# Kernel tuning notes

Hardware: AMD Instinct MI355X
Metric: run time of the kernel (lower is better)

## Reference

```python
import jax, jax.numpy as jnp
import numpy as np

IN_DIM = 64
HIDDEN = 128
NUM_LAYERS = 2
N_NODES = 10000
N_EDGES = 160000
N_GRAPHS = 32


def _lin_params(key, fan_in, fan_out):
    kw, kb = jax.random.split(key)
    s = 1.0 / np.sqrt(fan_in)
    W = jax.random.uniform(kw, (fan_in, fan_out), jnp.float32, -s, s)
    b = jax.random.uniform(kb, (fan_out,), jnp.float32, -s, s)
    return W, b


def setup_inputs() -> dict:
    key = jax.random.key(0)
    ks = jax.random.split(key, 24)
    H = HIDDEN
    inp = {}
    inp["x1"] = jax.random.normal(ks[0], (N_NODES, IN_DIM), jnp.float32)
    inp["edge_index1"] = jax.random.randint(ks[1], (2, N_EDGES), 0, N_NODES)
    inp["batch1"] = jnp.sort(jax.random.randint(ks[2], (N_NODES,), 0, N_GRAPHS))
    inp["x2"] = jax.random.normal(ks[3], (N_NODES, IN_DIM), jnp.float32)
    inp["edge_index2"] = jax.random.randint(ks[4], (2, N_EDGES), 0, N_NODES)
    inp["batch2"] = jnp.sort(jax.random.randint(ks[5], (N_NODES,), 0, N_GRAPHS))
    # embedding: Linear(in_dim -> hidden)
    inp["W_emb"], inp["b_emb"] = _lin_params(ks[6], IN_DIM, H)
    # per-layer GEMBConv params, stacked over layers
    mW1, mb1, mW2, mb2, uW1, ub1, uW2, ub2 = [], [], [], [], [], [], [], []
    for l in range(NUM_LAYERS):
        k = jax.random.split(ks[7 + l], 4)
        W, b = _lin_params(k[0], 2 * H, 2 * H); mW1.append(W); mb1.append(b)
        W, b = _lin_params(k[1], 2 * H, 2 * H); mW2.append(W); mb2.append(b)
        W, b = _lin_params(k[2], 3 * H, 2 * H); uW1.append(W); ub1.append(b)
        W, b = _lin_params(k[3], 2 * H, H); uW2.append(W); ub2.append(b)
    inp["msg_W1"] = jnp.stack(mW1); inp["msg_b1"] = jnp.stack(mb1)
    inp["msg_W2"] = jnp.stack(mW2); inp["msg_b2"] = jnp.stack(mb2)
    inp["upd_W1"] = jnp.stack(uW1); inp["upd_b1"] = jnp.stack(ub1)
    inp["upd_W2"] = jnp.stack(uW2); inp["upd_b2"] = jnp.stack(ub2)
    # readout: node_net Linear(H -> 2H) (use_gate doubles), graph_net Linear(H -> H)
    inp["node_W"], inp["node_b"] = _lin_params(ks[20], H, 2 * H)
    inp["graph_W"], inp["graph_b"] = _lin_params(ks[21], H, H)
    return inp


def _genet_branch(x, edge_index, batch, W_emb, b_emb,
                  msg_W1, msg_b1, msg_W2, msg_b2,
                  upd_W1, upd_b1, upd_W2, upd_b2,
                  node_W, node_b, graph_W, graph_b):
    H = HIDDEN
    h = x @ W_emb + b_emb  # [N, H]
    tgt, src = edge_index[0], edge_index[1]
    for l in range(NUM_LAYERS):
        # gather-concat: (x[src], x[tgt]) -> [E, 2H]
        mi = jnp.concatenate([h[src], h[tgt]], axis=-1)
        m = jax.nn.relu(mi @ msg_W1[l] + msg_b1[l]) @ msg_W2[l] + msg_b2[l]
        agg = jax.ops.segment_sum(m, tgt, num_segments=N_NODES)  # [N, 2H]
        ui = jnp.concatenate([agg, h], axis=-1)  # [N, 3H]
        u = jax.nn.relu(ui @ upd_W1[l] + upd_b1[l]) @ upd_W2[l] + upd_b2[l]
        h = h + u  # residual node update
    nx = h @ node_W + node_b  # [N, 2H]
    gates = jax.nn.sigmoid(nx[:, :H])
    v = nx[:, H:] * gates
    g = jax.ops.segment_sum(v, batch, num_segments=N_GRAPHS)  # sum pool
    return g @ graph_W + graph_b  # [G, H]


def reference(x1, edge_index1, batch1, x2, edge_index2, batch2,
              W_emb, b_emb, msg_W1, msg_b1, msg_W2, msg_b2,
              upd_W1, upd_b1, upd_W2, upd_b2,
              node_W, node_b, graph_W, graph_b):
    args = (W_emb, b_emb, msg_W1, msg_b1, msg_W2, msg_b2,
            upd_W1, upd_b1, upd_W2, upd_b2, node_W, node_b, graph_W, graph_b)
    embed1 = _genet_branch(x1, edge_index1, batch1, *args)
    embed2 = _genet_branch(x2, edge_index2, batch2, *args)
    return (embed1, embed2)
```

## Files before the change

### kernel.cpp

```cpp
#include <hip/hip_runtime.h>

typedef unsigned short u16;
typedef __bf16 bf16x8 __attribute__((ext_vector_type(8)));
typedef float f32x4 __attribute__((ext_vector_type(4)));
typedef unsigned short u16x8 __attribute__((ext_vector_type(8)));

constexpr int NN  = 10000;
constexpr int NE  = 160000;
constexpr int NG  = 32;
constexpr int HD  = 128;

constexpr size_t WT_PQ   = 0;
constexpr size_t WT_U1C  = 917504;
constexpr size_t WT_UPD2 = 1310720;
constexpr size_t WT_NODE = 1441792;
constexpr size_t OFF_C2  = 1507328;
constexpr size_t OFF_DEG = 1509376;
constexpr size_t OFF_ST  = 1589376;
constexpr size_t OFF_CUR = 1669440;
constexpr size_t OFF_SRC = 1749440;
constexpr size_t OFF_H   = 3029440;
constexpr size_t OFF_HB  = 13269440;
constexpr size_t OFF_PQ  = 18389440;
constexpr size_t OFF_UI  = 38869440;
constexpr size_t OFF_G   = 54229440;
constexpr size_t OFF_XB  = 54262208;
constexpr size_t WT_EMB  = 56822208;

#define LSTR 40

__device__ inline u16 f2b(float f) {
  unsigned int u = __float_as_uint(f);
  unsigned int r = u + 0x7fffu + ((u >> 16) & 1u);
  return (u16)(r >> 16);
}
__device__ inline float b2f(u16 u) { return __uint_as_float(((unsigned int)u) << 16); }

__global__ __launch_bounds__(256) void k_prep(
    const float* msgW1, const float* msgW2, const float* updW1,
    const float* updW2, const float* nodeW, const float* msgb2,
    const float* W_emb, const float* x1, const float* x2,
    u16* tpq, u16* tu1c, u16* t4, u16* t5, u16* temb, u16* xb,
    float* c2, int* deg, float* g) {
  int idx = blockIdx.x * 256 + threadIdx.x;
  if (idx < 131072) {
    int l = idx >> 16, r = idx & 65535, n = r >> 7, k = r & 127;
    int row = (n < 256) ? k : (128 + k);
    tpq[idx] = f2b(msgW1[l * 65536 + row * 256 + (n & 255)]);
  }
  if (idx < 65536) {
    int l = idx >> 15, r = idx & 32767, n = r >> 7, k = r & 127;
    tu1c[l * 98304 + n * 384 + 256 + k] = f2b(updW1[l * 98304 + (256 + k) * 256 + n]);
    int n2 = (idx & 32767) >> 8, k2 = idx & 255;
    t4[idx] = f2b(updW2[(idx >> 15) * 32768 + (k2 << 7) + n2]);
  }
  if (idx < 32768) {
    int n = idx >> 7, k = idx & 127;
    t5[idx] = f2b(nodeW[(k << 8) + n]);
  }
  if (idx < 512) {
    int l = idx >> 8, n = idx & 255;
    const float* b2 = msgb2 + l * 256;
    const float* U1 = updW1 + l * 98304 + n;
    float a = 0.f;
    for (int c = 0; c < 256; c++) a += b2[c] * U1[c * 256];
    c2[idx] = a;
  }
  if (idx < 2 * NN) deg[idx] = 0;
  if (idx < 2 * NG * 128) g[idx] = 0.f;
  if (idx >= 131072 && idx < 262144) {
    int j = idx - 131072;
    int l = j >> 16, r = j & 65535, k = r >> 8, n = r & 255;
    const float* w2p = msgW2 + l * 65536 + k * 256;
    const float* u1p = updW1 + l * 98304 + n;
    float a = 0.f;
    for (int c = 0; c < 256; c++) a += w2p[c] * u1p[c * 256];
    tu1c[l * 98304 + n * 384 + k] = f2b(a);
  }
  if (idx >= 262144 && idx < 270336) {
    int j = idx - 262144;
    int n = j >> 6, k = j & 63;
    temb[j] = f2b(W_emb[(k << 7) + n]);
  }
  if (idx >= 270336 && idx < 1550336) {
    int j = idx - 270336;
    int br = j >= NN * 64;
    int jj = br ? j - NN * 64 : j;
    const float* x = br ? x2 : x1;
    xb[(size_t)br * NN * 64 + jj] = f2b(x[jj]);
  }
}

__global__ __launch_bounds__(256) void k_deg(const int* ei0, const int* ei1, int* deg) {
  int br = blockIdx.z;
  int e = blockIdx.x * 256 + threadIdx.x;
  if (e >= NE) return;
  const int* tgt = br ? ei1 : ei0;
  atomicAdd(deg + br * NN + tgt[e], 1);
}

__global__ __launch_bounds__(256) void k_scan(const int* deg, int* starts, int* cursor) {
  int br = blockIdx.z;
  const int* d = deg + br * NN;
  int* st = starts + br * (NN + 8);
  int* cu = cursor + br * NN;
  __shared__ int part[257];
  int t = threadIdx.x;
  int c0 = t * 40;
  int s = 0;
  for (int i = 0; i < 40; i++) if (c0 + i < NN) s += d[c0 + i];
  part[t] = s;
  __syncthreads();
  if (t == 0) {
    int run = 0;
    for (int i = 0; i < 256; i++) { int v = part[i]; part[i] = run; run += v; }
    part[256] = run;
  }
  __syncthreads();
  int run = part[t];
  for (int i = 0; i < 40; i++) {
    int n = c0 + i;
    if (n < NN) { st[n] = run; cu[n] = run; run += d[n]; }
  }
  if (t == 255) st[NN] = part[256];
}

__global__ __launch_bounds__(256) void k_scatter(const int* ei0, const int* ei1,
                                                 int* cursor, int* srcs) {
  int br = blockIdx.z;
  int e = blockIdx.x * 256 + threadIdx.x;
  if (e >= NE) return;
  const int* ei = br ? ei1 : ei0;
  int t = ei[e], s = ei[NE + e];
  int pos = atomicAdd(cursor + br * NN + t, 1);
  srcs[br * NE + pos] = s;
}

__device__ __forceinline__ void pq_from_lhb(
    const u16* lhb, const u16* wq, u16* PQ, int m0, int wave, int lane) {
  const int q = lane >> 4, lr = lane & 15;
  f32x4 a3[2][8];
#pragma unroll
  for (int i = 0; i < 2; i++)
#pragma unroll
    for (int j = 0; j < 8; j++) a3[i][j] = (f32x4){0.f, 0.f, 0.f, 0.f};
  bf16x8 bcur[8], bnxt[8];
#pragma unroll
  for (int i = 0; i < 8; i++)
    bcur[i] = *(const bf16x8*)(wq + (size_t)(wave * 128 + i * 16 + lr) * 128 + q * 8);
#pragma unroll
  for (int k0 = 0; k0 < 128; k0 += 32) {
    if (k0 + 32 < 128) {
#pragma unroll
      for (int i = 0; i < 8; i++)
        bnxt[i] = *(const bf16x8*)(wq + (size_t)(wave * 128 + i * 16 + lr) * 128 + k0 + 32 + q * 8);
    }
    bf16x8 af[2];
#pragma unroll
    for (int i = 0; i < 2; i++)
      af[i] = *(const bf16x8*)&lhb[(i * 16 + lr) * 136 + k0 + q * 8];
#pragma unroll
    for (int mi = 0; mi < 2; mi++)
#pragma unroll
      for (int ni = 0; ni < 8; ni++)
        a3[mi][ni] = __builtin_amdgcn_mfma_f32_16x16x32_bf16(af[mi], bcur[ni], a3[mi][ni], 0, 0, 0);
#pragma unroll
    for (int i = 0; i < 8; i++) bcur[i] = bnxt[i];
  }
#pragma unroll
  for (int mi = 0; mi < 2; mi++)
#pragma unroll
    for (int rg = 0; rg < 4; rg++) {
      int grow = m0 + mi * 16 + q * 4 + rg;
      if (grow >= NN) continue;
#pragma unroll
      for (int ni = 0; ni < 8; ni++) {
        int col = wave * 128 + ni * 16 + lr;
        PQ[(size_t)grow * 512 + col] = f2b(a3[mi][ni][rg]);
      }
    }
}

__global__ __launch_bounds__(256) void k_embed(
    const u16* xb_all, const u16* wemb, const float* b,
    float* h, u16* h_bf, u16* ui, const u16* wpq0, u16* PQ_all) {
  const int br = blockIdx.z;
  const int tid = threadIdx.x;
  const int lane = tid & 63, wave = tid >> 6;
  const int q = lane >> 4, lr = lane & 15;
  const int m0 = blockIdx.x * 32;

  __shared__ alignas(16) u16 lx[32 * 72];
  __shared__ alignas(16) u16 lhb[32 * 136];

  const u16* xb = xb_all + (size_t)br * NN * 64;
  {
    int r = tid >> 3, kc = (tid & 7) * 8;
    int gr = m0 + r;
    u16x8 v = {0, 0, 0, 0, 0, 0, 0, 0};
    if (gr < NN) v = *(const u16x8*)(xb + (size_t)gr * 64 + kc);
    *(u16x8*)&lx[r * 72 + kc] = v;
  }
  __syncthreads();

  const int wn = wave * 32;
  f32x4 acc[2][2];
#pragma unroll
  for (int i = 0; i < 2; i++)
#pragma unroll
    for (int j = 0; j < 2; j++) acc[i][j] = (f32x4){0.f, 0.f, 0.f, 0.f};

#pragma unroll
  for (int k0 = 0; k0 < 64; k0 += 32) {
    bf16x8 af[2], bfr[2];
#pragma unroll
    for (int i = 0; i < 2; i++)
      af[i] = *(const bf16x8*)&lx[(i * 16 + lr) * 72 + k0 + q * 8];
#pragma unroll
    for (int i = 0; i < 2; i++)
      bfr[i] = *(const bf16x8*)(wemb + (size_t)(wn + i * 16 + lr) * 64 + k0 + q * 8);
#pragma unroll
    for (int mi = 0; mi < 2; mi++)
#pragma unroll
      for (int ni = 0; ni < 2; ni++)
        acc[mi][ni] = __builtin_amdgcn_mfma_f32_16x16x32_bf16(af[mi], bfr[ni], acc[mi][ni], 0, 0, 0);
  }

  float* hB = h + (size_t)br * NN * HD;
  u16* hbB = h_bf + (size_t)br * NN * HD;
  u16* uiB = ui + (size_t)br * NN * 384;
#pragma unroll
  for (int mi = 0; mi < 2; mi++)
#pragma unroll
    for (int rg = 0; rg < 4; rg++) {
      int lrow = mi * 16 + q * 4 + rg;
      int gr = m0 + lrow;
#pragma unroll
      for (int ni = 0; ni < 2; ni++) {
        int col = wn + ni * 16 + lr;
        if (gr < NN) {
          float nh = acc[mi][ni][rg] + b[col];
          u16 bv = f2b(nh);
          hB[(size_t)gr * HD + col] = nh;
          hbB[(size_t)gr * HD + col] = bv;
          uiB[(size_t)gr * 384 + 256 + col] = bv;
          lhb[lrow * 136 + col] = bv;
        } else {
          lhb[lrow * 136 + col] = 0;
        }
      }
    }
  __syncthreads();
  pq_from_lhb(lhb, wpq0, PQ_all + (size_t)br * NN * 512, m0, wave, lane);
}

__global__ __launch_bounds__(256) void k_edge(const u16* PQ, const int* starts,
                                              const int* srcs, const float* b1, u16* ui) {
  int br = blockIdx.z;
  int node = blockIdx.x * 4 + (threadIdx.x >> 6);
  int lane = threadIdx.x & 63;
  int half = lane >> 5;
  int c0 = (lane & 31) * 8;
  const u16* PQb = PQ + (size_t)br * NN * 512;
  const int* st = starts + br * (NN + 8);
  const int* sr = srcs + br * NE;
  u16x8 qr = *(const u16x8*)(PQb + (size_t)node * 512 + 256 + c0);
  float qv[8], acc[8];
#pragma unroll
  for (int j = 0; j < 8; j++) { qv[j] = b2f(qr[j]) + b1[c0 + j]; acc[j] = 0.f; }
  int e0 = st[node], e1 = st[node + 1];
  int mid = e0 + ((e1 - e0 + 1) >> 1);
  int e = half ? mid : e0;
  int ee = half ? e1 : mid;
  for (; e + 3 < ee; e += 4) {
    int s0 = sr[e], s1 = sr[e + 1], s2 = sr[e + 2], s3 = sr[e + 3];
    u16x8 p0 = *(const u16x8*)(PQb + (size_t)s0 * 512 + c0);
    u16x8 p1 = *(const u16x8*)(PQb + (size_t)s1 * 512 + c0);
    u16x8 p2 = *(const u16x8*)(PQb + (size_t)s2 * 512 + c0);
    u16x8 p3 = *(const u16x8*)(PQb + (size_t)s3 * 512 + c0);
#pragma unroll
    for (int j = 0; j < 8; j++) {
      float v0 = b2f(p0[j]) + qv[j];
      float v1 = b2f(p1[j]) + qv[j];
      float v2 = b2f(p2[j]) + qv[j];
      float v3 = b2f(p3[j]) + qv[j];
      acc[j] += (v0 > 0.f ? v0 : 0.f) + (v1 > 0.f ? v1 : 0.f)
              + (v2 > 0.f ? v2 : 0.f) + (v3 > 0.f ? v3 : 0.f);
    }
  }
  for (; e + 1 < ee; e += 2) {
    int s0 = sr[e], s1 = sr[e + 1];
    u16x8 p0 = *(const u16x8*)(PQb + (size_t)s0 * 512 + c0);
    u16x8 p1 = *(const u16x8*)(PQb + (size_t)s1 * 512 + c0);
#pragma unroll
    for (int j = 0; j < 8; j++) {
      float v0 = b2f(p0[j]) + qv[j];
      float v1 = b2f(p1[j]) + qv[j];
      acc[j] += (v0 > 0.f ? v0 : 0.f) + (v1 > 0.f ? v1 : 0.f);
    }
  }
  if (e < ee) {
    int s0 = sr[e];
    u16x8 p0 = *(const u16x8*)(PQb + (size_t)s0 * 512 + c0);
#pragma unroll
    for (int j = 0; j < 8; j++) {
      float v0 = b2f(p0[j]) + qv[j];
      acc[j] += (v0 > 0.f ? v0 : 0.f);
    }
  }
#pragma unroll
  for (int j = 0; j < 8; j++) acc[j] += __shfl_xor(acc[j], 32);
  if (half == 0) {
    u16x8 o;
#pragma unroll
    for (int j = 0; j < 8; j++) o[j] = f2b(acc[j]);
    *(u16x8*)(ui + (size_t)br * NN * 384 + (size_t)node * 384 + c0) = o;
  }
}

__global__ __launch_bounds__(256, 4) void k_upd(
    const u16* ui_all, const u16* w1c, const float* b1u, const float* c2l,
    const int* deg_all, const u16* w2, const float* b2u,
    float* h_all, u16* hb_all, int mode,
    const u16* wpq_next, u16* PQ_all,
    const u16* wnode, const float* nb, const int* b0v, const int* b1v, float* g) {
  const int br = blockIdx.z;
  const int tid = threadIdx.x;
  const int lane = tid & 63, wave = tid >> 6;
  const int q = lane >> 4, lr = lane & 15;
  const int m0 = blockIdx.x * 32;

  __shared__ alignas(16) u16 lA[32 * 392];
  __shared__ alignas(16) u16 lhb[32 * 136];
  __shared__ int sbat[32];
  u16* lU = lA;

  const u16* ui = ui_all + (size_t)br * NN * 384;

  for (int c = tid; c < 1536; c += 256) {
    int r = c / 48, kc = (c % 48) * 8;
    int gr = m0 + r;
    u16x8 v = {0, 0, 0, 0, 0, 0, 0, 0};
    if (gr < NN) v = *(const u16x8*)(ui + (size_t)gr * 384 + kc);
    *(u16x8*)&lA[r * 392 + kc] = v;
  }
  if (mode == 1 && tid < 32) {
    const int* batch = br ? b1v : b0v;
    int n = m0 + tid;
    sbat[tid] = (n < NN) ? batch[n] : -1;
  }
  __syncthreads();

  const int wn = wave * 64;
  f32x4 acc[2][4];
#pragma unroll
  for (int i = 0; i < 2; i++)
#pragma unroll
    for (int j = 0; j < 4; j++) acc[i][j] = (f32x4){0.f, 0.f, 0.f, 0.f};

  bf16x8 bcur[4], bnxt[4];
#pragma unroll
  for (int i = 0; i < 4; i++)
    bcur[i] = *(const bf16x8*)(w1c + (size_t)(wn + i * 16 + lr) * 384 + q * 8);
#pragma unroll
  for (int k0 = 0; k0 < 384; k0 += 32) {
    if (k0 + 32 < 384) {
#pragma unroll
      for (int i = 0; i < 4; i++)
        bnxt[i] = *(const bf16x8*)(w1c + (size_t)(wn + i * 16 + lr) * 384 + k0 + 32 + q * 8);
    }
    bf16x8 af[2];
#pragma unroll
    for (int i = 0; i < 2; i++)
      af[i] = *(const bf16x8*)&lA[(i * 16 + lr) * 392 + k0 + q * 8];
#pragma unroll
    for (int mi = 0; mi < 2; mi++)
#pragma unroll
      for (int ni = 0; ni < 4; ni++)
        acc[mi][ni] = __builtin_amdgcn_mfma_f32_16x16x32_bf16(af[mi], bcur[ni], acc[mi][ni], 0, 0, 0);
#pragma unroll
    for (int i = 0; i < 4; i++) bcur[i] = bnxt[i];
  }
  __syncthreads();

  const int* deg = deg_all + br * NN;
#pragma unroll
  for (int mi = 0; mi < 2; mi++)
#pragma unroll
    for (int rg = 0; rg < 4; rg++) {
      int row = mi * 16 + q * 4 + rg;
      int gr = m0 + row;
      float d = (gr < NN) ? (float)deg[gr] : 0.f;
#pragma unroll
      for (int ni = 0; ni < 4; ni++) {
        int col = wn + ni * 16 + lr;
        float v = acc[mi][ni][rg] + b1u[col] + d * c2l[col];
        if (v < 0.f) v = 0.f;
        lU[row * 272 + col] = f2b(v);
      }
    }
  __syncthreads();

  const int wn2 = wave * 32;
  f32x4 acc2[2][2];
#pragma unroll
  for (int i = 0; i < 2; i++)
#pragma unroll
    for (int j = 0; j < 2; j++) acc2[i][j] = (f32x4){0.f, 0.f, 0.f, 0.f};

  bf16x8 b2c[2], b2n[2];
#pragma unroll
  for (int i = 0; i < 2; i++)
    b2c[i] = *(const bf16x8*)(w2 + (size_t)(wn2 + i * 16 + lr) * 256 + q * 8);
#pragma unroll
  for (int k0 = 0; k0 < 256; k0 += 32) {
    if (k0 + 32 < 256) {
#pragma unroll
      for (int i = 0; i < 2; i++)
        b2n[i] = *(const bf16x8*)(w2 + (size_t)(wn2 + i * 16 + lr) * 256 + k0 + 32 + q * 8);
    }
    bf16x8 af[2];
#pragma unroll
    for (int i = 0; i < 2; i++)
      af[i] = *(const bf16x8*)&lU[(i * 16 + lr) * 272 + k0 + q * 8];
#pragma unroll
    for (int mi = 0; mi < 2; mi++)
#pragma unroll
      for (int ni = 0; ni < 2; ni++)
        acc2[mi][ni] = __builtin_amdgcn_mfma_f32_16x16x32_bf16(af[mi], b2c[ni], acc2[mi][ni], 0, 0, 0);
#pragma unroll
    for (int i = 0; i < 2; i++) b2c[i] = b2n[i];
  }

  float* h = h_all + (size_t)br * NN * 128;
  u16* hb = hb_all + (size_t)br * NN * 128;
  u16* uiw = (u16*)ui_all + (size_t)br * NN * 384;
#pragma unroll
  for (int mi = 0; mi < 2; mi++)
#pragma unroll
    for (int rg = 0; rg < 4; rg++) {
      int lrow = mi * 16 + q * 4 + rg;
      int grow = m0 + lrow;
#pragma unroll
      for (int ni = 0; ni < 2; ni++) {
        int col = wn2 + ni * 16 + lr;
        if (grow < NN) {
          size_t o = (size_t)grow * 128 + col;
          float nh = h[o] + acc2[mi][ni][rg] + b2u[col];
          u16 bv = f2b(nh);
          h[o] = nh;
          hb[o] = bv;
          uiw[(size_t)grow * 384 + 256 + col] = bv;
          lhb[lrow * 136 + col] = bv;
        } else {
          lhb[lrow * 136 + col] = 0;
        }
      }
    }
  __syncthreads();

  if (mode == 0) {
    pq_from_lhb(lhb, wpq_next, PQ_all + (size_t)br * NN * 512, m0, wave, lane);
  } else {
    const int wg = wave * 32;
    f32x4 a3[2][4];
#pragma unroll
    for (int i = 0; i < 2; i++)
#pragma unroll
      for (int j = 0; j < 4; j++) a3[i][j] = (f32x4){0.f, 0.f, 0.f, 0.f};
#pragma unroll
    for (int k0 = 0; k0 < 128; k0 += 32) {
      bf16x8 af[2], bfr[4];
#pragma unroll
      for (int i = 0; i < 2; i++)
        af[i] = *(const bf16x8*)&lhb[(i * 16 + lr) * 136 + k0 + q * 8];
#pragma unroll
      for (int i = 0; i < 4; i++) {
        int nrow = (i < 2) ? (wg + i * 16 + lr) : (128 + wg + (i - 2) * 16 + lr);
        bfr[i] = *(const bf16x8*)(wnode + (size_t)nrow * 128 + k0 + q * 8);
      }
#pragma unroll
      for (int mi = 0; mi < 2; mi++)
#pragma unroll
        for (int ni = 0; ni < 4; ni++)
          a3[mi][ni] = __builtin_amdgcn_mfma_f32_16x16x32_bf16(af[mi], bfr[ni], a3[mi][ni], 0, 0, 0);
    }
    float* gb = g + (size_t)br * NG * 128;
    float racc[2] = {0.f, 0.f};
    int cur = -1;
#pragma unroll
    for (int mi = 0; mi < 2; mi++)
#pragma unroll
      for (int rg = 0; rg < 4; rg++) {
        int lrow = mi * 16 + q * 4 + rg;
        int bt = sbat[lrow];
        if (bt != cur) {
          if (cur >= 0) {
#pragma unroll
            for (int ni = 0; ni < 2; ni++)
              atomicAdd(gb + (size_t)cur * 128 + wg + ni * 16 + lr, racc[ni]);
          }
          cur = bt;
          racc[0] = 0.f; racc[1] = 0.f;
        }
        if (bt >= 0) {
#pragma unroll
          for (int ni = 0; ni < 2; ni++) {
            int gcol = wg + ni * 16 + lr;
            float gt = a3[mi][ni][rg] + nb[gcol];
            float vl = a3[mi][ni + 2][rg] + nb[128 + gcol];
            racc[ni] += vl / (1.f + __expf(-gt));
          }
        }
      }
    if (cur >= 0) {
#pragma unroll
      for (int ni = 0; ni < 2; ni++)
        atomicAdd(gb + (size_t)cur * 128 + wg + ni * 16 + lr, racc[ni]);
    }
  }
}

__global__ __launch_bounds__(128) void k_final(const float* g, const float* W,
                                               const float* b, float* out) {
  int br = blockIdx.z, gi = blockIdx.x, j = threadIdx.x;
  __shared__ float sg[128];
  sg[j] = g[(size_t)br * NG * 128 + (size_t)gi * 128 + j];
  __syncthreads();
  float acc = b[j];
#pragma unroll
  for (int k = 0; k < 128; k++) acc += sg[k] * W[k * 128 + j];
  out[(size_t)br * NG * 128 + (size_t)gi * 128 + j] = acc;
}

extern "C" void kernel_launch(void* const* d_in, const int* in_sizes, int n_in,
                              void* d_out, int out_size, void* d_ws, size_t ws_size,
                              hipStream_t stream) {
  const float* x1     = (const float*)d_in[0];
  const int*   ei1    = (const int*)d_in[1];
  const int*   bat1   = (const int*)d_in[2];
  const float* x2     = (const float*)d_in[3];
  const int*   ei2    = (const int*)d_in[4];
  const int*   bat2   = (const int*)d_in[5];
  const float* W_emb  = (const float*)d_in[6];
  const float* b_emb  = (const float*)d_in[7];
  const float* msg_W1 = (const float*)d_in[8];
  const float* msg_b1 = (const float*)d_in[9];
  const float* msg_W2 = (const float*)d_in[10];
  const float* msg_b2 = (const float*)d_in[11];
  const float* upd_W1 = (const float*)d_in[12];
  const float* upd_b1 = (const float*)d_in[13];
  const float* upd_W2 = (const float*)d_in[14];
  const float* upd_b2 = (const float*)d_in[15];
  const float* node_W = (const float*)d_in[16];
  const float* node_b = (const float*)d_in[17];
  const float* graph_W = (const float*)d_in[18];
  const float* graph_b = (const float*)d_in[19];
  float* out = (float*)d_out;

  char* ws = (char*)d_ws;
  u16* wt_pq   = (u16*)(ws + WT_PQ);
  u16* wt_u1c  = (u16*)(ws + WT_U1C);
  u16* wt_upd2 = (u16*)(ws + WT_UPD2);
  u16* wt_node = (u16*)(ws + WT_NODE);
  u16* wt_emb  = (u16*)(ws + WT_EMB);
  u16* xb      = (u16*)(ws + OFF_XB);
  float* c2    = (float*)(ws + OFF_C2);
  int* deg    = (int*)(ws + OFF_DEG);
  int* starts = (int*)(ws + OFF_ST);
  int* cursor = (int*)(ws + OFF_CUR);
  int* srcs   = (int*)(ws + OFF_SRC);
  float* h  = (float*)(ws + OFF_H);
  u16*   hb = (u16*)(ws + OFF_HB);
  u16*   PQ = (u16*)(ws + OFF_PQ);
  u16*   ui = (u16*)(ws + OFF_UI);
  float* g  = (float*)(ws + OFF_G);

  k_prep<<<6057, 256, 0, stream>>>(msg_W1, msg_W2, upd_W1, upd_W2, node_W, msg_b2,
                                   W_emb, x1, x2,
                                   wt_pq, wt_u1c, wt_upd2, wt_node, wt_emb, xb,
                                   c2, deg, g);
  k_deg<<<dim3(625, 1, 2), 256, 0, stream>>>(ei1, ei2, deg);
  k_scan<<<dim3(1, 1, 2), 256, 0, stream>>>(deg, starts, cursor);
  k_scatter<<<dim3(625, 1, 2), 256, 0, stream>>>(ei1, ei2, cursor, srcs);
  k_embed<<<dim3(313, 1, 2), 256, 0, stream>>>(xb, wt_emb, b_emb, h, hb, ui,
                                               wt_pq, PQ);

  for (int l = 0; l < 2; l++) {
    k_edge<<<dim3(2500, 1, 2), 256, 0, stream>>>(PQ, starts, srcs, msg_b1 + l * 256, ui);

    k_upd<<<dim3(313, 1, 2), 256, 0, stream>>>(
        ui, wt_u1c + (size_t)l * 98304, upd_b1 + l * 256, c2 + l * 256,
        deg, wt_upd2 + (size_t)l * 32768, upd_b2 + l * 128, h, hb,
        (l == 0) ? 0 : 1,
        wt_pq + 65536, PQ,
        wt_node, node_b, bat1, bat2, g);
  }

  k_final<<<dim3(NG, 1, 2), 128, 0, stream>>>(g, graph_W, graph_b, out);
}
```

Before: 331.8 us.

## Split node update into tiled GEMM kernel plus fused second-stage kernel

Result: slower. 345.9 us (+4.2%).

```diff
diff --git a/kernel.cpp b/kernel.cpp
--- a/kernel.cpp
+++ b/kernel.cpp
@@ -26,6 +26,7 @@
 constexpr size_t OFF_G   = 54229440;
 constexpr size_t OFF_XB  = 54262208;
 constexpr size_t WT_EMB  = 56822208;
+constexpr size_t OFF_U1  = 56838592;
 
 #define LSTR 40
 
@@ -144,28 +145,20 @@
   for (int i = 0; i < 2; i++)
 #pragma unroll
     for (int j = 0; j < 8; j++) a3[i][j] = (f32x4){0.f, 0.f, 0.f, 0.f};
-  bf16x8 bcur[8], bnxt[8];
-#pragma unroll
-  for (int i = 0; i < 8; i++)
-    bcur[i] = *(const bf16x8*)(wq + (size_t)(wave * 128 + i * 16 + lr) * 128 + q * 8);
 #pragma unroll
   for (int k0 = 0; k0 < 128; k0 += 32) {
-    if (k0 + 32 < 128) {
-#pragma unroll
-      for (int i = 0; i < 8; i++)
-        bnxt[i] = *(const bf16x8*)(wq + (size_t)(wave * 128 + i * 16 + lr) * 128 + k0 + 32 + q * 8);
-    }
-    bf16x8 af[2];
+    bf16x8 af[2], bfr[8];
 #pragma unroll
     for (int i = 0; i < 2; i++)
       af[i] = *(const bf16x8*)&lhb[(i * 16 + lr) * 136 + k0 + q * 8];
 #pragma unroll
+    for (int i = 0; i < 8; i++)
+      bfr[i] = *(const bf16x8*)(wq + (size_t)(wave * 128 + i * 16 + lr) * 128 + k0 + q * 8);
+#pragma unroll
     for (int mi = 0; mi < 2; mi++)
 #pragma unroll
       for (int ni = 0; ni < 8; ni++)
-        a3[mi][ni] = __builtin_amdgcn_mfma_f32_16x16x32_bf16(af[mi], bcur[ni], a3[mi][ni], 0, 0, 0);
-#pragma unroll
-    for (int i = 0; i < 8; i++) bcur[i] = bnxt[i];
+        a3[mi][ni] = __builtin_amdgcn_mfma_f32_16x16x32_bf16(af[mi], bfr[ni], a3[mi][ni], 0, 0, 0);
   }
 #pragma unroll
   for (int mi = 0; mi < 2; mi++)
@@ -318,93 +311,107 @@
   }
 }
 
-__global__ __launch_bounds__(256, 4) void k_upd(
+__global__ __launch_bounds__(256) void k_upd1(
     const u16* ui_all, const u16* w1c, const float* b1u, const float* c2l,
-    const int* deg_all, const u16* w2, const float* b2u,
-    float* h_all, u16* hb_all, int mode,
+    const int* deg_all, u16* U1_all) {
+  const int br = blockIdx.z;
+  const int tid = threadIdx.x;
+  const int lane = tid & 63, wave = tid >> 6;
+  const int wm = (wave & 1) * 64, wn = (wave >> 1) * 64;
+  const int q = lane >> 4, lr = lane & 15;
+  const int m0 = blockIdx.x * 128, n0 = blockIdx.y * 128;
+  __shared__ alignas(16) u16 lA[128 * LSTR];
+  __shared__ alignas(16) u16 lB[128 * LSTR];
+
+  f32x4 acc[4][4];
+#pragma unroll
+  for (int i = 0; i < 4; i++)
+#pragma unroll
+    for (int j = 0; j < 4; j++) acc[i][j] = (f32x4){0.f, 0.f, 0.f, 0.f};
+
+  const u16* ui = ui_all + (size_t)br * NN * 384;
+
+  for (int k0 = 0; k0 < 384; k0 += 32) {
+#pragma unroll
+    for (int c = tid; c < 512; c += 256) {
+      int r = c >> 2, kc = (c & 3) << 3;
+      int gr = m0 + r;
+      u16x8 v = {0, 0, 0, 0, 0, 0, 0, 0};
+      if (gr < NN) v = *(const u16x8*)(ui + (size_t)gr * 384 + k0 + kc);
+      *(u16x8*)&lA[r * LSTR + kc] = v;
+    }
+#pragma unroll
+    for (int c = tid; c < 512; c += 256) {
+      int r = c >> 2, kc = (c & 3) << 3;
+      *(u16x8*)&lB[r * LSTR + kc] = *(const u16x8*)(w1c + (size_t)(n0 + r) * 384 + k0 + kc);
+    }
+    __syncthreads();
+    bf16x8 af[4], bfr[4];
+#pragma unroll
+    for (int i = 0; i < 4; i++) af[i] = *(const bf16x8*)&lA[(wm + i * 16 + lr) * LSTR + q * 8];
+#pragma unroll
+    for (int i = 0; i < 4; i++) bfr[i] = *(const bf16x8*)&lB[(wn + i * 16 + lr) * LSTR + q * 8];
+#pragma unroll
+    for (int mi = 0; mi < 4; mi++)
+#pragma unroll
+      for (int ni = 0; ni < 4; ni++)
+        acc[mi][ni] = __builtin_amdgcn_mfma_f32_16x16x32_bf16(af[mi], bfr[ni], acc[mi][ni], 0, 0, 0);
+    __syncthreads();
+  }
+
+  const int* deg = deg_all + br * NN;
+  u16* U1 = U1_all + (size_t)br * NN * 256;
+#pragma unroll
+  for (int mi = 0; mi < 4; mi++)
+#pragma unroll
+    for (int rg = 0; rg < 4; rg++) {
+      int row = m0 + wm + mi * 16 + q * 4 + rg;
+      if (row >= NN) continue;
+      float d = (float)deg[row];
+#pragma unroll
+      for (int ni = 0; ni < 4; ni++) {
+        int col = n0 + wn + ni * 16 + lr;
+        float v = acc[mi][ni][rg] + b1u[col] + d * c2l[col];
+        if (v < 0.f) v = 0.f;
+        U1[(size_t)row * 256 + col] = f2b(v);
+      }
+    }
+}
+
+__global__ __launch_bounds__(256, 3) void k_upd2(
+    const u16* U1_all, const u16* w2, const float* b2u,
+    float* h_all, u16* hb_all, u16* ui_all, int mode,
     const u16* wpq_next, u16* PQ_all,
     const u16* wnode, const float* nb, const int* b0v, const int* b1v, float* g) {
   const int br = blockIdx.z;
   const int tid = threadIdx.x;
   const int lane = tid & 63, wave = tid >> 6;
   const int q = lane >> 4, lr = lane & 15;
-  const int m0 = blockIdx.x * 32;
-
-  __shared__ alignas(16) u16 lA[32 * 392];
-  __shared__ alignas(16) u16 lhb[32 * 136];
-  __shared__ int sbat[32];
-  u16* lU = lA;
-
-  const u16* ui = ui_all + (size_t)br * NN * 384;
-
-  for (int c = tid; c < 1536; c += 256) {
-    int r = c / 48, kc = (c % 48) * 8;
+  const int m0 = blockIdx.x * 64;
+
+  __shared__ alignas(16) u16 lU[64 * 264];
+  __shared__ alignas(16) u16 lhb[64 * 136];
+  __shared__ int sbat[64];
+
+  const u16* U1 = U1_all + (size_t)br * NN * 256;
+  for (int c = tid; c < 2048; c += 256) {
+    int r = c >> 5, kc = (c & 31) * 8;
     int gr = m0 + r;
     u16x8 v = {0, 0, 0, 0, 0, 0, 0, 0};
-    if (gr < NN) v = *(const u16x8*)(ui + (size_t)gr * 384 + kc);
-    *(u16x8*)&lA[r * 392 + kc] = v;
-  }
-  if (mode == 1 && tid < 32) {
+    if (gr < NN) v = *(const u16x8*)(U1 + (size_t)gr * 256 + kc);
+    *(u16x8*)&lU[r * 264 + kc] = v;
+  }
+  if (mode == 1 && tid < 64) {
     const int* batch = br ? b1v : b0v;
     int n = m0 + tid;
     sbat[tid] = (n < NN) ? batch[n] : -1;
   }
   __syncthreads();
 
-  const int wn = wave * 64;
-  f32x4 acc[2][4];
-#pragma unroll
-  for (int i = 0; i < 2; i++)
-#pragma unroll
-    for (int j = 0; j < 4; j++) acc[i][j] = (f32x4){0.f, 0.f, 0.f, 0.f};
-
-  bf16x8 bcur[4], bnxt[4];
+  const int wn2 = wave * 32;
+  f32x4 acc2[4][2];
 #pragma unroll
   for (int i = 0; i < 4; i++)
-    bcur[i] = *(const bf16x8*)(w1c + (size_t)(wn + i * 16 + lr) * 384 + q * 8);
-#pragma unroll
-  for (int k0 = 0; k0 < 384; k0 += 32) {
-    if (k0 + 32 < 384) {
-#pragma unroll
-      for (int i = 0; i < 4; i++)
-        bnxt[i] = *(const bf16x8*)(w1c + (size_t)(wn + i * 16 + lr) * 384 + k0 + 32 + q * 8);
-    }
-    bf16x8 af[2];
-#pragma unroll
-    for (int i = 0; i < 2; i++)
-      af[i] = *(const bf16x8*)&lA[(i * 16 + lr) * 392 + k0 + q * 8];
-#pragma unroll
-    for (int mi = 0; mi < 2; mi++)
-#pragma unroll
-      for (int ni = 0; ni < 4; ni++)
-        acc[mi][ni] = __builtin_amdgcn_mfma_f32_16x16x32_bf16(af[mi], bcur[ni], acc[mi][ni], 0, 0, 0);
-#pragma unroll
-    for (int i = 0; i < 4; i++) bcur[i] = bnxt[i];
-  }
-  __syncthreads();
-
-  const int* deg = deg_all + br * NN;
-#pragma unroll
-  for (int mi = 0; mi < 2; mi++)
-#pragma unroll
-    for (int rg = 0; rg < 4; rg++) {
-      int row = mi * 16 + q * 4 + rg;
-      int gr = m0 + row;
-      float d = (gr < NN) ? (float)deg[gr] : 0.f;
-#pragma unroll
-      for (int ni = 0; ni < 4; ni++) {
-        int col = wn + ni * 16 + lr;
-        float v = acc[mi][ni][rg] + b1u[col] + d * c2l[col];
-        if (v < 0.f) v = 0.f;
-        lU[row * 272 + col] = f2b(v);
-      }
-    }
-  __syncthreads();
-
-  const int wn2 = wave * 32;
-  f32x4 acc2[2][2];
-#pragma unroll
-  for (int i = 0; i < 2; i++)
 #pragma unroll
     for (int j = 0; j < 2; j++) acc2[i][j] = (f32x4){0.f, 0.f, 0.f, 0.f};
 
@@ -419,12 +426,12 @@
       for (int i = 0; i < 2; i++)
         b2n[i] = *(const bf16x8*)(w2 + (size_t)(wn2 + i * 16 + lr) * 256 + k0 + 32 + q * 8);
     }
-    bf16x8 af[2];
-#pragma unroll
-    for (int i = 0; i < 2; i++)
-      af[i] = *(const bf16x8*)&lU[(i * 16 + lr) * 272 + k0 + q * 8];
-#pragma unroll
-    for (int mi = 0; mi < 2; mi++)
+    bf16x8 af[4];
+#pragma unroll
+    for (int i = 0; i < 4; i++)
+      af[i] = *(const bf16x8*)&lU[(i * 16 + lr) * 264 + k0 + q * 8];
+#pragma unroll
+    for (int mi = 0; mi < 4; mi++)
 #pragma unroll
       for (int ni = 0; ni < 2; ni++)
         acc2[mi][ni] = __builtin_amdgcn_mfma_f32_16x16x32_bf16(af[mi], b2c[ni], acc2[mi][ni], 0, 0, 0);
@@ -434,9 +441,9 @@
 
   float* h = h_all + (size_t)br * NN * 128;
   u16* hb = hb_all + (size_t)br * NN * 128;
-  u16* uiw = (u16*)ui_all + (size_t)br * NN * 384;
-#pragma unroll
-  for (int mi = 0; mi < 2; mi++)
+  u16* uiw = ui_all + (size_t)br * NN * 384;
+#pragma unroll
+  for (int mi = 0; mi < 4; mi++)
 #pragma unroll
     for (int rg = 0; rg < 4; rg++) {
       int lrow = mi * 16 + q * 4 + rg;
@@ -450,7 +457,7 @@
           u16 bv = f2b(nh);
           h[o] = nh;
           hb[o] = bv;
-          uiw[(size_t)grow * 384 + 256 + col] = bv;
+          if (mode == 0) uiw[(size_t)grow * 384 + 256 + col] = bv;
           lhb[lrow * 136 + col] = bv;
         } else {
           lhb[lrow * 136 + col] = 0;
@@ -460,19 +467,55 @@
   __syncthreads();
 
   if (mode == 0) {
-    pq_from_lhb(lhb, wpq_next, PQ_all + (size_t)br * NN * 512, m0, wave, lane);
+    u16* PQ = PQ_all + (size_t)br * NN * 512;
+#pragma unroll
+    for (int nh = 0; nh < 2; nh++) {
+      f32x4 a3[4][4];
+#pragma unroll
+      for (int i = 0; i < 4; i++)
+#pragma unroll
+        for (int j = 0; j < 4; j++) a3[i][j] = (f32x4){0.f, 0.f, 0.f, 0.f};
+#pragma unroll
+      for (int k0 = 0; k0 < 128; k0 += 32) {
+        bf16x8 af[4], bfr[4];
+#pragma unroll
+        for (int i = 0; i < 4; i++)
+          af[i] = *(const bf16x8*)&lhb[(i * 16 + lr) * 136 + k0 + q * 8];
+#pragma unroll
+        for (int i = 0; i < 4; i++)
+          bfr[i] = *(const bf16x8*)(wpq_next +
+              (size_t)(wave * 128 + nh * 64 + i * 16 + lr) * 128 + k0 + q * 8);
+#pragma unroll
+        for (int mi = 0; mi < 4; mi++)
+#pragma unroll
+          for (int ni = 0; ni < 4; ni++)
+            a3[mi][ni] = __builtin_amdgcn_mfma_f32_16x16x32_bf16(af[mi], bfr[ni], a3[mi][ni], 0, 0, 0);
+      }
+#pragma unroll
+      for (int mi = 0; mi < 4; mi++)
+#pragma unroll
+        for (int rg = 0; rg < 4; rg++) {
+          int grow = m0 + mi * 16 + q * 4 + rg;
+          if (grow >= NN) continue;
+#pragma unroll
+          for (int ni = 0; ni < 4; ni++) {
+            int col = wave * 128 + nh * 64 + ni * 16 + lr;
+            PQ[(size_t)grow * 512 + col] = f2b(a3[mi][ni][rg]);
+          }
+        }
+    }
   } else {
     const int wg = wave * 32;
-    f32x4 a3[2][4];
-#pragma unroll
-    for (int i = 0; i < 2; i++)
+    f32x4 a3[4][4];
+#pragma unroll
+    for (int i = 0; i < 4; i++)
 #pragma unroll
       for (int j = 0; j < 4; j++) a3[i][j] = (f32x4){0.f, 0.f, 0.f, 0.f};
 #pragma unroll
     for (int k0 = 0; k0 < 128; k0 += 32) {
-      bf16x8 af[2], bfr[4];
-#pragma unroll
-      for (int i = 0; i < 2; i++)
+      bf16x8 af[4], bfr[4];
+#pragma unroll
+      for (int i = 0; i < 4; i++)
         af[i] = *(const bf16x8*)&lhb[(i * 16 + lr) * 136 + k0 + q * 8];
 #pragma unroll
       for (int i = 0; i < 4; i++) {
@@ -480,7 +523,7 @@
         bfr[i] = *(const bf16x8*)(wnode + (size_t)nrow * 128 + k0 + q * 8);
       }
 #pragma unroll
-      for (int mi = 0; mi < 2; mi++)
+      for (int mi = 0; mi < 4; mi++)
 #pragma unroll
         for (int ni = 0; ni < 4; ni++)
           a3[mi][ni] = __builtin_amdgcn_mfma_f32_16x16x32_bf16(af[mi], bfr[ni], a3[mi][ni], 0, 0, 0);
@@ -489,7 +532,7 @@
     float racc[2] = {0.f, 0.f};
     int cur = -1;
 #pragma unroll
-    for (int mi = 0; mi < 2; mi++)
+    for (int mi = 0; mi < 4; mi++)
 #pragma unroll
       for (int rg = 0; rg < 4; rg++) {
         int lrow = mi * 16 + q * 4 + rg;
@@ -574,6 +617,7 @@
   u16*   hb = (u16*)(ws + OFF_HB);
   u16*   PQ = (u16*)(ws + OFF_PQ);
   u16*   ui = (u16*)(ws + OFF_UI);
+  u16*   U1 = (u16*)(ws + OFF_U1);
   float* g  = (float*)(ws + OFF_G);
 
   k_prep<<<6057, 256, 0, stream>>>(msg_W1, msg_W2, upd_W1, upd_W2, node_W, msg_b2,
@@ -589,9 +633,11 @@
   for (int l = 0; l < 2; l++) {
     k_edge<<<dim3(2500, 1, 2), 256, 0, stream>>>(PQ, starts, srcs, msg_b1 + l * 256, ui);
 
-    k_upd<<<dim3(313, 1, 2), 256, 0, stream>>>(
-        ui, wt_u1c + (size_t)l * 98304, upd_b1 + l * 256, c2 + l * 256,
-        deg, wt_upd2 + (size_t)l * 32768, upd_b2 + l * 128, h, hb,
+    k_upd1<<<dim3(79, 2, 2), 256, 0, stream>>>(
+        ui, wt_u1c + (size_t)l * 98304, upd_b1 + l * 256, c2 + l * 256, deg, U1);
+
+    k_upd2<<<dim3(157, 1, 2), 256, 0, stream>>>(
+        U1, wt_upd2 + (size_t)l * 32768, upd_b2 + l * 128, h, hb, ui,
         (l == 0) ? 0 : 1,
         wt_pq + 65536, PQ,
         wt_node, node_b, bat1, bat2, g);
```
